# Kernel tuning notes

Hardware: AMD Instinct MI355X
Metric: run time of the kernel (lower is better)

## Reference

```python
import jax, jax.numpy as jnp
import numpy as np

TEMPERATURE = 0.5


def setup_inputs() -> dict:
    key = jax.random.key(0)
    k1, k2 = jax.random.split(key)
    N, D = 4096, 256
    z_i = jax.random.normal(k1, (N, D), dtype=jnp.float32)
    z_j = jax.random.normal(k2, (N, D), dtype=jnp.float32)
    return {"z_i": z_i, "z_j": z_j}


def reference(z_i, z_j):
    N = z_i.shape[0]
    z = jnp.concatenate([z_i, z_j], axis=0)            # (2N, D)
    sim = (z @ z.T) / TEMPERATURE                       # (2N, 2N)
    # mask self-similarity on the diagonal
    diag = jnp.eye(2 * N, dtype=bool)
    sim = jnp.where(diag, -jnp.inf, sim)
    # positive pair labels: i <-> i+N
    labels = jnp.concatenate([jnp.arange(N, 2 * N), jnp.arange(0, N)])
    logp = jax.nn.log_softmax(sim, axis=-1)             # (2N, 2N)
    loss = -jnp.mean(jnp.take_along_axis(logp, labels[:, None], axis=-1))
    return loss
```

## Files before the change

### kernel.cpp

```cpp
#include <hip/hip_runtime.h>
#include <hip/hip_bf16.h>


typedef __bf16 bf16x8 __attribute__((ext_vector_type(8)));
typedef __bf16 bf16x4 __attribute__((ext_vector_type(4)));
typedef float  f32x16 __attribute__((ext_vector_type(16)));

#define NPAIR 4096
#define NROW  8192
#define DIM   256
#define STRIPS 16
#define RBLK  16384
#define SQSCALE 1.6986437f
#define LN2F    0.6931471805599453f
#define M2      176.0f

__global__ __launch_bounds__(256) void k_convert(const float* __restrict__ zi,
                                                 const float* __restrict__ zj,
                                                 __bf16* __restrict__ Zf,
                                                 float* __restrict__ pos,
                                                 float* __restrict__ out) {
    const int w = threadIdx.x >> 6, lane = threadIdx.x & 63;
    const int r = blockIdx.x * 4 + w;
    if (blockIdx.x == 0 && threadIdx.x == 0) out[0] = 0.0f;
    const float4 vi = *(const float4*)(zi + r * DIM + lane * 4);
    const float4 vj = *(const float4*)(zj + r * DIM + lane * 4);
    bf16x4 bi, bj;
    bi[0] = (__bf16)(vi.x * SQSCALE); bi[1] = (__bf16)(vi.y * SQSCALE);
    bi[2] = (__bf16)(vi.z * SQSCALE); bi[3] = (__bf16)(vi.w * SQSCALE);
    bj[0] = (__bf16)(vj.x * SQSCALE); bj[1] = (__bf16)(vj.y * SQSCALE);
    bj[2] = (__bf16)(vj.z * SQSCALE); bj[3] = (__bf16)(vj.w * SQSCALE);
    const int t = lane >> 2, h = (lane >> 1) & 1, inner = (lane & 1) * 8;
    char* Zb = (char*)Zf;
    *(bf16x4*)(Zb + (size_t)(r >> 5) * RBLK + t * 1024 + h * 512 + (r & 31) * 16 + inner) = bi;
    const int r2 = r + NPAIR;
    *(bf16x4*)(Zb + (size_t)(r2 >> 5) * RBLK + t * 1024 + h * 512 + (r2 & 31) * 16 + inner) = bj;
    float d = vi.x * vj.x + vi.y * vj.y + vi.z * vj.z + vi.w * vj.w;
    #pragma unroll
    for (int m = 32; m >= 1; m >>= 1) d += __shfl_xor(d, m);
    if (lane == 0) pos[r] = 2.0f * d;
}

__global__ __launch_bounds__(256, 2) void k_lse(const __bf16* __restrict__ Zf,
                                                float* __restrict__ Lpart) {
    const int bx    = blockIdx.x;
    const int rb    = bx & 31;
    const int strip = bx >> 5;
    const int tid   = threadIdx.x;
    const int w     = tid >> 6;
    const int lane  = tid & 63, lm = lane & 31, half = lane >> 5;
    const int laneoff = half * 512 + lm * 16;
    const int R0 = rb * 8 + w * 2, R1 = R0 + 1;

    __shared__ __align__(16) char smem[65536];
    const char* Zb = (const char*)Zf;

    bf16x8 B0[16], B1[16];
    {
        const char* g0 = Zb + (size_t)R0 * RBLK + laneoff;
        const char* g1 = Zb + (size_t)R1 * RBLK + laneoff;
        #pragma unroll
        for (int t = 0; t < 16; t++) {
            B0[t] = *(const bf16x8*)(g0 + t * 1024);
            B1[t] = *(const bf16x8*)(g1 + t * 1024);
        }
    }
    #pragma unroll
    for (int t = 0; t < 16; t++) {
        asm volatile("" : "+v"(B0[t]));
        asm volatile("" : "+v"(B1[t]));
    }

    const char* Acol = Zb + (size_t)strip * 16 * RBLK;

    #define STAGE(bufsel, phidx) do {                                              \
        const char* _s = Acol + (size_t)(phidx) * RBLK + tid * 16;                 \
        char*       _d = smem + (bufsel) * 16384 + tid * 16;                       \
        _Pragma("unroll")                                                          \
        for (int _q = 0; _q < 4; _q++)                                             \
            __builtin_amdgcn_global_load_lds(                                      \
                (const __attribute__((address_space(1))) unsigned int*)(_s + _q * 4096), \
                (__attribute__((address_space(3))) unsigned int*)(_d + _q * 4096), \
                16, 0, 0);                                                         \
    } while (0)

    float l0 = 0.0f, l1 = 0.0f;

    #define PHASE_BODY(PH, WAITSTR, DO_STAGE) do {                                 \
        asm volatile("s_waitcnt vmcnt(" WAITSTR ")" ::: "memory");                 \
        __builtin_amdgcn_s_barrier();                                              \
        asm volatile("" ::: "memory");                                             \
        if (DO_STAGE) STAGE(((PH) + 3) & 3, (PH) + 3);                             \
        const char* Ab = smem + ((PH) & 3) * 16384 + laneoff;                      \
        f32x16 acc0 = (f32x16)(0.0f);                                              \
        f32x16 acc1 = (f32x16)(0.0f);                                              \
        __builtin_amdgcn_s_setprio(1);                                             \
        _Pragma("unroll")                                                          \
        for (int t = 0; t < 16; t++) {                                             \
            bf16x8 a = *(const bf16x8*)(Ab + t * 1024);                            \
            acc0 = __builtin_amdgcn_mfma_f32_32x32x16_bf16(a, B0[t], acc0, 0, 0, 0); \
            acc1 = __builtin_amdgcn_mfma_f32_32x32x16_bf16(a, B1[t], acc1, 0, 0, 0); \
        }                                                                          \
        __builtin_amdgcn_s_setprio(0);                                             \
        const int cb = strip * 16 + (PH);                                          \
        if (cb == R0) {            \
            _Pragma("unroll")                                                      \
            for (int rg = 0; rg < 16; rg++) {                                      \
                const int cl = (rg & 3) + 8 * (rg >> 2) + 4 * half;                \
                acc0[rg] = (cl == lm) ? -1e30f : acc0[rg];                         \
            }                                                                      \
        }                                                                          \
        if (cb == R1) {                                                            \
            _Pragma("unroll")                                                      \
            for (int rg = 0; rg < 16; rg++) {                                      \
                const int cl = (rg & 3) + 8 * (rg >> 2) + 4 * half;                \
                acc1[rg] = (cl == lm) ? -1e30f : acc1[rg];                         \
            }                                                                      \
        }                                                                          \
        float p0 = 0.0f, p1 = 0.0f, q0 = 0.0f, q1 = 0.0f;                          \
        _Pragma("unroll")                                                          \
        for (int rg = 0; rg < 16; rg += 2) {                                       \
            p0 += __builtin_exp2f(acc0[rg]     - M2);                              \
            p1 += __builtin_exp2f(acc0[rg + 1] - M2);                              \
            q0 += __builtin_exp2f(acc1[rg]     - M2);                              \
            q1 += __builtin_exp2f(acc1[rg + 1] - M2);                              \
        }                                                                          \
        l0 += p0 + p1;                                                             \
        l1 += q0 + q1;                                                             \
    } while (0)

    STAGE(0, 0);
    STAGE(1, 1);
    STAGE(2, 2);

    for (int ph = 0; ph < 14; ph++) {
        PHASE_BODY(ph, "8", ph < 13);
    }
    PHASE_BODY(14, "4", 0);
    PHASE_BODY(15, "0", 0);

    #undef PHASE_BODY
    #undef STAGE

    l0 += __shfl_xor(l0, 32);
    l1 += __shfl_xor(l1, 32);
    if (half == 0) {
        Lpart[strip * NROW + R0 * 32 + lm] = l0;
        Lpart[strip * NROW + R1 * 32 + lm] = l1;
    }
}

__global__ __launch_bounds__(256) void k_final(const float* __restrict__ Lpart,
                                               const float* __restrict__ pos,
                                               float* __restrict__ out) {
    __shared__ float red[256];
    const int t = threadIdx.x;
    const int r = blockIdx.x * 256 + t;
    float l = 0.0f;
    #pragma unroll
    for (int s = 0; s < STRIPS; s++) l += Lpart[s * NROW + r];
    const float lse = (M2 + __builtin_log2f(l)) * LN2F;
    red[t] = lse - pos[r & (NPAIR - 1)];
    __syncthreads();
    for (int ofs = 128; ofs > 0; ofs >>= 1) {
        if (t < ofs) red[t] += red[t + ofs];
        __syncthreads();
    }
    if (t == 0) atomicAdd(out, red[0] / (float)NROW);
}

extern "C" void kernel_launch(void* const* d_in, const int* in_sizes, int n_in,
                              void* d_out, int out_size, void* d_ws, size_t ws_size,
                              hipStream_t stream) {
    const float* zi = (const float*)d_in[0];
    const float* zj = (const float*)d_in[1];
    __bf16* Zf   = (__bf16*)d_ws;
    float* pos   = (float*)((char*)d_ws + (size_t)NROW * DIM * 2);
    float* Lpart = pos + NPAIR;

    k_convert<<<NPAIR / 4, 256, 0, stream>>>(zi, zj, Zf, pos, (float*)d_out);
    k_lse<<<32 * STRIPS, 256, 0, stream>>>(Zf, Lpart);
    k_final<<<NROW / 256, 256, 0, stream>>>(Lpart, pos, (float*)d_out);
}
```

Before: 100.5 us.

## Process two column blocks per phase with double-buffered LDS staging

Restructures the main loop from 16 phases over four single-block LDS buffers into 8 phases that each process two 32-column blocks from a double buffer. Each phase now issues four MFMA chains instead of two, and the masking and exp-sum logic is updated to match. The intent is to halve the number of barriers and raise independent MFMA work per phase. In exchange, prefetch depth drops to one phase ahead, with a full vmcnt(0) wait each phase. The change also swaps in the raw amdgcn exp2 builtin and removes the asm register pinning of the B fragments.

```diff
diff --git a/kernel.cpp b/kernel.cpp
--- a/kernel.cpp
+++ b/kernel.cpp
@@ -14,6 +14,8 @@
 #define SQSCALE 1.6986437f
 #define LN2F    0.6931471805599453f
 #define M2      176.0f
+
+#define EXP2F(x) __builtin_amdgcn_exp2f(x)
 
 __global__ __launch_bounds__(256) void k_convert(const float* __restrict__ zi,
                                                  const float* __restrict__ zj,
@@ -65,82 +67,79 @@
             B1[t] = *(const bf16x8*)(g1 + t * 1024);
         }
     }
-    #pragma unroll
-    for (int t = 0; t < 16; t++) {
-        asm volatile("" : "+v"(B0[t]));
-        asm volatile("" : "+v"(B1[t]));
-    }
 
     const char* Acol = Zb + (size_t)strip * 16 * RBLK;
 
-    #define STAGE(bufsel, phidx) do {                                              \
-        const char* _s = Acol + (size_t)(phidx) * RBLK + tid * 16;                 \
-        char*       _d = smem + (bufsel) * 16384 + tid * 16;                       \
+    #define STAGE2(phidx) do {                                                     \
         _Pragma("unroll")                                                          \
-        for (int _q = 0; _q < 4; _q++)                                             \
-            __builtin_amdgcn_global_load_lds(                                      \
-                (const __attribute__((address_space(1))) unsigned int*)(_s + _q * 4096), \
-                (__attribute__((address_space(3))) unsigned int*)(_d + _q * 4096), \
-                16, 0, 0);                                                         \
+        for (int _r = 0; _r < 2; _r++) {                                           \
+            const char* _s = Acol + (size_t)(2 * (phidx) + _r) * RBLK + tid * 16;  \
+            char*       _d = smem + ((phidx) & 1) * 32768 + _r * 16384 + tid * 16; \
+            _Pragma("unroll")                                                      \
+            for (int _q = 0; _q < 4; _q++)                                         \
+                __builtin_amdgcn_global_load_lds(                                  \
+                    (const __attribute__((address_space(1))) unsigned int*)(_s + _q * 4096), \
+                    (__attribute__((address_space(3))) unsigned int*)(_d + _q * 4096), \
+                    16, 0, 0);                                                     \
+        }                                                                          \
     } while (0)
 
     float l0 = 0.0f, l1 = 0.0f;
 
-    #define PHASE_BODY(PH, WAITSTR, DO_STAGE) do {                                 \
-        asm volatile("s_waitcnt vmcnt(" WAITSTR ")" ::: "memory");                 \
+    #define PHASE_BODY(PH, DO_STAGE) do {                                          \
+        asm volatile("s_waitcnt vmcnt(0)" ::: "memory");                           \
         __builtin_amdgcn_s_barrier();                                              \
         asm volatile("" ::: "memory");                                             \
-        if (DO_STAGE) STAGE(((PH) + 3) & 3, (PH) + 3);                             \
-        const char* Ab = smem + ((PH) & 3) * 16384 + laneoff;                      \
-        f32x16 acc0 = (f32x16)(0.0f);                                              \
-        f32x16 acc1 = (f32x16)(0.0f);                                              \
+        if (DO_STAGE) STAGE2((PH) + 1);                                            \
+        const char* Ab0 = smem + ((PH) & 1) * 32768 + laneoff;                     \
+        const char* Ab1 = Ab0 + 16384;                                             \
+        f32x16 acc00 = (f32x16)(0.0f);                      \
+        f32x16 acc01 = (f32x16)(0.0f);                      \
+        f32x16 acc10 = (f32x16)(0.0f);                      \
+        f32x16 acc11 = (f32x16)(0.0f);                      \
         __builtin_amdgcn_s_setprio(1);                                             \
         _Pragma("unroll")                                                          \
         for (int t = 0; t < 16; t++) {                                             \
-            bf16x8 a = *(const bf16x8*)(Ab + t * 1024);                            \
-            acc0 = __builtin_amdgcn_mfma_f32_32x32x16_bf16(a, B0[t], acc0, 0, 0, 0); \
-            acc1 = __builtin_amdgcn_mfma_f32_32x32x16_bf16(a, B1[t], acc1, 0, 0, 0); \
+            bf16x8 a0 = *(const bf16x8*)(Ab0 + t * 1024);                          \
+            bf16x8 a1 = *(const bf16x8*)(Ab1 + t * 1024);                          \
+            acc00 = __builtin_amdgcn_mfma_f32_32x32x16_bf16(a0, B0[t], acc00, 0, 0, 0); \
+            acc01 = __builtin_amdgcn_mfma_f32_32x32x16_bf16(a0, B1[t], acc01, 0, 0, 0); \
+            acc10 = __builtin_amdgcn_mfma_f32_32x32x16_bf16(a1, B0[t], acc10, 0, 0, 0); \
+            acc11 = __builtin_amdgcn_mfma_f32_32x32x16_bf16(a1, B1[t], acc11, 0, 0, 0); \
         }                                                                          \
         __builtin_amdgcn_s_setprio(0);                                             \
-        const int cb = strip * 16 + (PH);                                          \
-        if (cb == R0) {            \
+        \
+        \
+        const int cb0 = strip * 16 + 2 * (PH);                                     \
+        if (cb0 == R0) {                                                           \
             _Pragma("unroll")                                                      \
             for (int rg = 0; rg < 16; rg++) {                                      \
                 const int cl = (rg & 3) + 8 * (rg >> 2) + 4 * half;                \
-                acc0[rg] = (cl == lm) ? -1e30f : acc0[rg];                         \
-            }                                                                      \
-        }                                                                          \
-        if (cb == R1) {                                                            \
-            _Pragma("unroll")                                                      \
-            for (int rg = 0; rg < 16; rg++) {                                      \
-                const int cl = (rg & 3) + 8 * (rg >> 2) + 4 * half;                \
-                acc1[rg] = (cl == lm) ? -1e30f : acc1[rg];                         \
+                acc00[rg] = (cl == lm) ? -1e30f : acc00[rg];                       \
+                acc11[rg] = (cl == lm) ? -1e30f : acc11[rg];                       \
             }                                                                      \
         }                                                                          \
         float p0 = 0.0f, p1 = 0.0f, q0 = 0.0f, q1 = 0.0f;                          \
         _Pragma("unroll")                                                          \
-        for (int rg = 0; rg < 16; rg += 2) {                                       \
-            p0 += __builtin_exp2f(acc0[rg]     - M2);                              \
-            p1 += __builtin_exp2f(acc0[rg + 1] - M2);                              \
-            q0 += __builtin_exp2f(acc1[rg]     - M2);                              \
-            q1 += __builtin_exp2f(acc1[rg + 1] - M2);                              \
+        for (int rg = 0; rg < 16; rg++) {                                          \
+            p0 += EXP2F(acc00[rg] - M2);                                           \
+            p1 += EXP2F(acc10[rg] - M2);                                           \
+            q0 += EXP2F(acc01[rg] - M2);                                           \
+            q1 += EXP2F(acc11[rg] - M2);                                           \
         }                                                                          \
         l0 += p0 + p1;                                                             \
         l1 += q0 + q1;                                                             \
     } while (0)
 
-    STAGE(0, 0);
-    STAGE(1, 1);
-    STAGE(2, 2);
+    STAGE2(0);
 
-    for (int ph = 0; ph < 14; ph++) {
-        PHASE_BODY(ph, "8", ph < 13);
+    for (int ph = 0; ph < 7; ph++) {
+        PHASE_BODY(ph, 1);
     }
-    PHASE_BODY(14, "4", 0);
-    PHASE_BODY(15, "0", 0);
+    PHASE_BODY(7, 0);
 
     #undef PHASE_BODY
-    #undef STAGE
+    #undef STAGE2
 
     l0 += __shfl_xor(l0, 32);
     l1 += __shfl_xor(l1, 32);
```

Result: no change. 98.70 us (-1.8%).
